# Performance work log

Hardware: AMD Instinct MI355X
Metric: run time of the kernel (lower is better)

Reference implementation:

```python
import jax, jax.numpy as jnp
import numpy as np

V, E, H, B, T = 50257, 300, 512, 4, 512  # vocab, embed(300 fixed), hid_size, batch, max_seq_len


def setup_inputs() -> dict:
    key = jax.random.key(0)
    ks = jax.random.split(key, 12)
    n = lambda k, shp, s: jax.random.normal(k, shp, dtype=jnp.float32) * s
    return {
        "tokens": jax.random.randint(ks[0], (B, T), 0, V),
        "emb_table": n(ks[1], (V, E), 0.02),      # frozen pretrained embedding
        # forward-direction LstmCellWithProjection params (cell_size == hidden_size == H)
        "W_ih_f": n(ks[2], (E, 4 * H), 0.05),     # input_linearity (no bias)
        "W_hh_f": n(ks[3], (H, 4 * H), 0.05),     # state_linearity weight
        "b_f": jnp.zeros((4 * H,), jnp.float32),  # state_linearity bias
        "W_proj_f": n(ks[4], (H, H), 0.05),       # state_projection (no bias)
        # backward direction
        "W_ih_b": n(ks[5], (E, 4 * H), 0.05),
        "W_hh_b": n(ks[6], (H, 4 * H), 0.05),
        "b_b": jnp.zeros((4 * H,), jnp.float32),
        "W_proj_b": n(ks[7], (H, H), 0.05),
        # final vocab projection nn.Linear(H, V)
        "W_lin": n(ks[8], (H, V), 0.02),
        "b_lin": jnp.zeros((V,), jnp.float32),
    }


def _lstm_proj_scan(x, W_ih, W_hh, b, W_proj):
    """ElmoLstm's LstmCellWithProjection over time. x: [B,T,E] -> [B,T,H]."""
    xp = jnp.einsum("bte,eg->btg", x, W_ih)  # precompute input projections [B,T,4H]

    def step(carry, xt):  # xt: [B,4H]
        h, c = carry
        p = xt + h @ W_hh + b
        i = jax.nn.sigmoid(p[:, :H])
        f = jax.nn.sigmoid(p[:, H:2 * H])
        g = jnp.tanh(p[:, 2 * H:3 * H])
        o = jax.nn.sigmoid(p[:, 3 * H:])
        c2 = i * g + f * c
        h2 = (o * jnp.tanh(c2)) @ W_proj  # projected hidden state
        return (h2, c2), h2

    init = (jnp.zeros((x.shape[0], H), x.dtype), jnp.zeros((x.shape[0], H), x.dtype))
    _, hs = jax.lax.scan(step, init, jnp.swapaxes(xp, 0, 1))  # [T,B,H]
    return jnp.swapaxes(hs, 0, 1)  # [B,T,H]


def reference(tokens, emb_table, W_ih_f, W_hh_f, b_f, W_proj_f,
              W_ih_b, W_hh_b, b_b, W_proj_b, W_lin, b_lin):
    x = emb_table[tokens]  # embedding gather [B,T,E]
    fwd = _lstm_proj_scan(x, W_ih_f, W_hh_f, b_f, W_proj_f)
    bwd = _lstm_proj_scan(x[:, ::-1], W_ih_b, W_hh_b, b_b, W_proj_b)[:, ::-1]
    # num_layers == 1 -> enc is (1,B,T,2H); fwd half / bwd half each through shared Linear
    logits_fwd = (fwd @ W_lin + b_lin).reshape(-1, V)  # [B*T, V]
    logits_bwd = (bwd @ W_lin + b_lin).reshape(-1, V)
    return jnp.concatenate([logits_fwd, logits_bwd], axis=0)  # [2*B*T, V]
```

## Files before the change

kernel.cpp:

```cpp
#include <hip/hip_runtime.h>
#include <hip/hip_bf16.h>

typedef unsigned short u16;
typedef unsigned int u32;
typedef unsigned long long u64;
typedef short bf16x8 __attribute__((ext_vector_type(8)));
typedef float f32x4 __attribute__((ext_vector_type(4)));

#define AS1C(p) ((const __attribute__((address_space(1))) void*)(p))
#define AS3(p)  ((__attribute__((address_space(3))) void*)(p))

__device__ __forceinline__ u16 f2bf(float f) {
    union { float f; unsigned u; } v; v.f = f;
    unsigned x = v.u;
    unsigned r = (x + 0x7FFFu + ((x >> 16) & 1u)) >> 16;
    return (u16)r;
}

__device__ __forceinline__ void tpose_dev(float (*tile)[33],
        const float* __restrict__ in, u16* __restrict__ out,
        int R, int C, int outR, int ldO, int bx, int by) {
    int c0 = bx * 32, r0 = by * 32;
    int tx = threadIdx.x & 31, ty = threadIdx.x >> 5;
#pragma unroll
    for (int yy = 0; yy < 4; ++yy) {
        int r = r0 + ty + yy * 8, cc = c0 + tx;
        tile[ty + yy * 8][tx] = (r < R && cc < C) ? in[(size_t)r * C + cc] : 0.f;
    }
    __syncthreads();
#pragma unroll
    for (int yy = 0; yy < 4; ++yy) {
        int c = c0 + ty + yy * 8, r = r0 + tx;
        if (c < outR && r < ldO) out[(size_t)c * ldO + r] = f2bf(tile[tx][ty + yy * 8]);
    }
}

__global__ __launch_bounds__(256) void prep(
    const int* __restrict__ tokens, const float* __restrict__ emb, u16* __restrict__ xemb,
    const float* __restrict__ W_ih_f, u16* __restrict__ WT_ihf,
    const float* __restrict__ W_ih_b, u16* __restrict__ WT_ihb,
    const float* __restrict__ W_hh_f, u16* __restrict__ WT_hhf,
    const float* __restrict__ W_hh_b, u16* __restrict__ WT_hhb,
    const float* __restrict__ W_proj_f, u16* __restrict__ WprojTf,
    const float* __restrict__ W_proj_b, u16* __restrict__ WprojTb,
    u16* __restrict__ WprojAf, u16* __restrict__ WprojAb,
    u64* __restrict__ htag)
{
    __shared__ float tile[32][33];
    int bid = blockIdx.x;
    int tid = threadIdx.x;
    if (bid < 2048) {
        int tok = tokens[bid];
        const float* src = emb + (size_t)tok * 300;
        u16* dst = xemb + (size_t)bid * 320;
        int c = tid;
        if (c < 320) dst[c] = (c < 300) ? f2bf(src[c]) : (u16)0;
        c += 256;
        if (c < 320) dst[c] = (c < 300) ? f2bf(src[c]) : (u16)0;
        return;
    }
    bid -= 2048;
    if (bid < 640)  { tpose_dev(tile, W_ih_f, WT_ihf, 300, 2048, 2048, 320, bid % 64, bid / 64); return; }
    bid -= 640;
    if (bid < 640)  { tpose_dev(tile, W_ih_b, WT_ihb, 300, 2048, 2048, 320, bid % 64, bid / 64); return; }
    bid -= 640;
    if (bid < 1024) { tpose_dev(tile, W_hh_f, WT_hhf, 512, 2048, 2048, 512, bid % 64, bid / 64); return; }
    bid -= 1024;
    if (bid < 1024) { tpose_dev(tile, W_hh_b, WT_hhb, 512, 2048, 2048, 512, bid % 64, bid / 64); return; }
    bid -= 1024;
    if (bid < 256)  { tpose_dev(tile, W_proj_f, WprojTf, 512, 512, 512, 512, bid % 16, bid / 16); return; }
    bid -= 256;
    if (bid < 256)  { tpose_dev(tile, W_proj_b, WprojTb, 512, 512, 512, 512, bid % 16, bid / 16); return; }
    bid -= 256;
    if (bid < 512)  { int i = bid * 512 + tid; WprojAf[i] = f2bf(W_proj_f[i]); WprojAf[i + 256] = f2bf(W_proj_f[i + 256]); return; }
    bid -= 512;
    if (bid < 512)  { int i = bid * 512 + tid; WprojAb[i] = f2bf(W_proj_b[i]); WprojAb[i + 256] = f2bf(W_proj_b[i + 256]); return; }
    bid -= 512;
    for (int i = tid; i < 2 * 2 * 4 * 256; i += 256) htag[i] = 0ull;
}

struct GemmJob {
    const u16* A; const u16* BT; float* Cf; u16* Cb; const float* bias;
    int M, Nreal, K, ldA, ldB, ldC, arev, orev, orow_base;
};

__device__ __forceinline__ void gemm_body(const GemmJob& j) {
    __shared__ char As[8192];
    __shared__ char Bs[8192];
    const int tid = threadIdx.x;
    const int lane = tid & 63;
    const int wid = tid >> 6;
    const int wr = wid >> 1, wc = wid & 1;
    const int m0 = blockIdx.y * 128;
    const int n0 = blockIdx.x * 128;

    f32x4 zero4 = {0.f, 0.f, 0.f, 0.f};
    f32x4 acc[4][4];
#pragma unroll
    for (int i = 0; i < 4; ++i)
#pragma unroll
        for (int jx = 0; jx < 4; ++jx) acc[i][jx] = zero4;

    const int kIters = j.K >> 5;
    const int l15 = lane & 15, kg = lane >> 4;

    const int srow0 = wid * 32 + (lane >> 2);
    const int srow1 = srow0 + 16;
    const int c0 = (lane & 3) ^ (srow0 & 3);
    const int c1 = (lane & 3) ^ (srow1 & 3);
    int ar0 = m0 + srow0, ar1 = m0 + srow1;
    if (j.arev) {
        ar0 = (ar0 & ~511) | (511 - (ar0 & 511));
        ar1 = (ar1 & ~511) | (511 - (ar1 & 511));
    }
    const u16* ga0 = j.A + (size_t)ar0 * j.ldA + c0 * 8;
    const u16* ga1 = j.A + (size_t)ar1 * j.ldA + c1 * 8;
    const u16* gb0 = j.BT + (size_t)(n0 + srow0) * j.ldB + c0 * 8;
    const u16* gb1 = j.BT + (size_t)(n0 + srow1) * j.ldB + c1 * 8;
    char* ldsA0 = As + wid * 2048;
    char* ldsA1 = As + wid * 2048 + 1024;
    char* ldsB0 = Bs + wid * 2048;
    char* ldsB1 = Bs + wid * 2048 + 1024;

    for (int kt = 0; kt < kIters; ++kt) {
        const int k0 = kt * 32;
        __builtin_amdgcn_global_load_lds(AS1C(ga0 + k0), AS3(ldsA0), 16, 0, 0);
        __builtin_amdgcn_global_load_lds(AS1C(ga1 + k0), AS3(ldsA1), 16, 0, 0);
        __builtin_amdgcn_global_load_lds(AS1C(gb0 + k0), AS3(ldsB0), 16, 0, 0);
        __builtin_amdgcn_global_load_lds(AS1C(gb1 + k0), AS3(ldsB1), 16, 0, 0);
        __syncthreads();

        bf16x8 af[4], bfr[4];
#pragma unroll
        for (int mt = 0; mt < 4; ++mt) {
            int r = wr * 64 + mt * 16 + l15;
            af[mt] = *(const bf16x8*)(As + r * 64 + ((kg ^ (r & 3)) * 16));
        }
#pragma unroll
        for (int nt = 0; nt < 4; ++nt) {
            int r = wc * 64 + nt * 16 + l15;
            bfr[nt] = *(const bf16x8*)(Bs + r * 64 + ((kg ^ (r & 3)) * 16));
        }
#pragma unroll
        for (int mt = 0; mt < 4; ++mt)
#pragma unroll
            for (int nt = 0; nt < 4; ++nt)
                acc[mt][nt] = __builtin_amdgcn_mfma_f32_16x16x32_bf16(af[mt], bfr[nt], acc[mt][nt], 0, 0, 0);
        __syncthreads();
    }

#pragma unroll
    for (int nt = 0; nt < 4; ++nt) {
        int col = n0 + wc * 64 + nt * 16 + l15;
        float bv = (j.bias != nullptr && col < j.Nreal) ? j.bias[col] : 0.f;
#pragma unroll
        for (int mt = 0; mt < 4; ++mt) {
#pragma unroll
            for (int jx = 0; jx < 4; ++jx) {
                int m = m0 + wr * 64 + mt * 16 + kg * 4 + jx;
                int om = j.orev ? ((m & ~511) | (511 - (m & 511))) : m;
                om += j.orow_base;
                if (col < j.Nreal) {
                    float v = acc[mt][nt][jx] + bv;
                    if (j.Cf) j.Cf[(size_t)om * j.ldC + col] = v;
                    else      j.Cb[(size_t)om * j.ldC + col] = f2bf(v);
                }
            }
        }
    }
}

__global__ __launch_bounds__(256) void gemm_multi4(GemmJob j0, GemmJob j1, GemmJob j2, GemmJob j3) {
    GemmJob j = (blockIdx.z == 0) ? j0 : (blockIdx.z == 1) ? j1 : (blockIdx.z == 2) ? j2 : j3;
    if ((int)blockIdx.y * 128 >= j.M) return;
    gemm_body(j);
}
__global__ __launch_bounds__(256) void gemm_multi2(GemmJob j0, GemmJob j1) {
    GemmJob j = blockIdx.z ? j1 : j0;
    gemm_body(j);
}
__global__ __launch_bounds__(256) void gemm_one(GemmJob j0) { gemm_body(j0); }

__global__ __launch_bounds__(256) void lstm_fused(
    const float* __restrict__ Wc_f, const float* __restrict__ Wc_b,
    const float* __restrict__ xp_f, const float* __restrict__ xp_b,
    u64* __restrict__ htag,
    u16* __restrict__ hpre_f, u16* __restrict__ hpre_b,
    const float* __restrict__ W_lin, u16* __restrict__ WT_lin)
{
    __shared__ float tile[32][33];
    __shared__ u16 hlds[4][520];
    __shared__ float gsum[4][4][16];
    __shared__ float cbuf[4][16];

    if (blockIdx.x >= 64) {
        int job = blockIdx.x - 64;
        tpose_dev(tile, W_lin, WT_lin, 512, 50257, 50304, 512, job % 1572, job / 1572);
        return;
    }
    __builtin_amdgcn_s_setprio(1);

    const int tid = threadIdx.x;
    const int dir = blockIdx.x >> 5;
    const int blk = blockIdx.x & 31;
    const int lane = tid & 63;
    const int wid = tid >> 6;
    const int l15 = lane & 15;
    const int kg = lane >> 4;

    const float* wcsrc = dir ? Wc_b : Wc_f;
    const float* xp    = dir ? xp_b : xp_f;
    u16* hpre          = dir ? hpre_b : hpre_f;
    u64* ht            = htag + (size_t)dir * 2 * 4 * 256;

    bf16x8 wcf[16];
#pragma unroll
    for (int ks = 0; ks < 16; ++ks) {
        bf16x8 w;
#pragma unroll
        for (int e = 0; e < 8; ++e) {
            int k = ks * 32 + kg * 8 + e;
            w[e] = (short)f2bf(wcsrc[(size_t)k * 2048 + wid * 512 + blk * 16 + l15]);
        }
        wcf[ks] = w;
    }
    if (tid < 64) cbuf[tid >> 4][tid & 15] = 0.f;
    __syncthreads();

    const bf16x8 zero8 = {0, 0, 0, 0, 0, 0, 0, 0};
    const int b = tid >> 4, hu = tid & 15;

    for (int t = 0; t < 512; ++t) {
        float xpv0 = 0.f, xpv1 = 0.f, xpv2 = 0.f, xpv3 = 0.f;
        if (tid < 64) {
            const float* xr = xp + ((size_t)(b * 512 + t)) * 2048 + blk * 16 + hu;
            xpv0 = xr[0]; xpv1 = xr[512]; xpv2 = xr[1024]; xpv3 = xr[1536];
        }
        {
            const u64* src = ht + (size_t)(t & 1) * 4 * 256;
            const u64* p0 = src + tid;
            const u64* p1 = src + 256 + tid;
            const u64* p2 = src + 512 + tid;
            const u64* p3 = src + 768 + tid;
            const u32 target = (u32)t;
            u64 w0, w1, w2, w3;
            for (;;) {
                asm volatile(
                    "global_load_dwordx2 %0, %4, off sc0 sc1\n\t"
                    "global_load_dwordx2 %1, %5, off sc0 sc1\n\t"
                    "global_load_dwordx2 %2, %6, off sc0 sc1\n\t"
                    "global_load_dwordx2 %3, %7, off sc0 sc1\n\t"
                    "s_waitcnt vmcnt(0)"
                    : "=&v"(w0), "=&v"(w1), "=&v"(w2), "=&v"(w3)
                    : "v"(p0), "v"(p1), "v"(p2), "v"(p3)
                    : "memory");
                if (((u32)(w0 >> 32) == target) & ((u32)(w1 >> 32) == target) &
                    ((u32)(w2 >> 32) == target) & ((u32)(w3 >> 32) == target)) break;
                __builtin_amdgcn_s_sleep(1);
            }
            asm volatile("" ::: "memory");
            *(u32*)&hlds[0][tid * 2] = (u32)w0;
            *(u32*)&hlds[1][tid * 2] = (u32)w1;
            *(u32*)&hlds[2][tid * 2] = (u32)w2;
            *(u32*)&hlds[3][tid * 2] = (u32)w3;
        }
        __syncthreads();

        f32x4 a0 = {0,0,0,0}, a1 = {0,0,0,0}, a2 = {0,0,0,0}, a3 = {0,0,0,0};
#pragma unroll
        for (int ks = 0; ks < 16; ++ks) {
            bf16x8 a = zero8;
            if (l15 < 4) a = *(const bf16x8*)&hlds[l15][ks * 32 + kg * 8];
            switch (ks & 3) {
                case 0: a0 = __builtin_amdgcn_mfma_f32_16x16x32_bf16(a, wcf[ks], a0, 0, 0, 0); break;
                case 1: a1 = __builtin_amdgcn_mfma_f32_16x16x32_bf16(a, wcf[ks], a1, 0, 0, 0); break;
                case 2: a2 = __builtin_amdgcn_mfma_f32_16x16x32_bf16(a, wcf[ks], a2, 0, 0, 0); break;
                default: a3 = __builtin_amdgcn_mfma_f32_16x16x32_bf16(a, wcf[ks], a3, 0, 0, 0); break;
            }
        }
        f32x4 accs = (a0 + a1) + (a2 + a3);
        if (lane < 16) {
#pragma unroll
            for (int jx = 0; jx < 4; ++jx) gsum[wid][jx][lane] = accs[jx];
        }
        __syncthreads();

        if (tid < 64) {
            float pi = xpv0 + gsum[0][b][hu];
            float pf = xpv1 + gsum[1][b][hu];
            float pg = xpv2 + gsum[2][b][hu];
            float po = xpv3 + gsum[3][b][hu];
            float iv = 1.f / (1.f + expf(-pi));
            float fv = 1.f / (1.f + expf(-pf));
            float gv = tanhf(pg);
            float ov = 1.f / (1.f + expf(-po));
            float c2 = iv * gv + fv * cbuf[b][hu];
            cbuf[b][hu] = c2;
            u16 hpb = f2bf(ov * tanhf(c2));
            unsigned v = hpb;
            unsigned nb = (unsigned)__shfl_down((int)v, 1);
            if ((tid & 1) == 0) {
                u32 packed = v | (nb << 16);
                u64 val = ((u64)(u32)(t + 1) << 32) | (u64)packed;
                size_t idx = (size_t)(((t + 1) & 1) * 4 + b) * 256 + blk * 8 + (hu >> 1);
                __hip_atomic_store(&ht[idx], val, __ATOMIC_RELAXED, __HIP_MEMORY_SCOPE_AGENT);
            }
            hpre[(size_t)(b * 512 + t) * 512 + blk * 16 + hu] = hpb;
        }
    }
}

extern "C" void kernel_launch(void* const* d_in, const int* in_sizes, int n_in,
                              void* d_out, int out_size, void* d_ws, size_t ws_size,
                              hipStream_t stream) {
    const int*   tokens   = (const int*)d_in[0];
    const float* emb      = (const float*)d_in[1];
    const float* W_ih_f   = (const float*)d_in[2];
    const float* W_hh_f   = (const float*)d_in[3];
    const float* b_f      = (const float*)d_in[4];
    const float* W_proj_f = (const float*)d_in[5];
    const float* W_ih_b   = (const float*)d_in[6];
    const float* W_hh_b   = (const float*)d_in[7];
    const float* b_b      = (const float*)d_in[8];
    const float* W_proj_b = (const float*)d_in[9];
    const float* W_lin    = (const float*)d_in[10];
    const float* b_lin    = (const float*)d_in[11];
    float* out = (float*)d_out;

    char* ws = (char*)d_ws;
    size_t off = 0;
    auto alloc = [&](size_t bytes) -> char* {
        char* p = ws + off;
        off = (off + bytes + 255) & ~(size_t)255;
        return p;
    };
    u16* xemb     = (u16*)alloc(2048 * 320 * 2);
    u16* WT_ihf   = (u16*)alloc(2048 * 320 * 2);
    u16* WT_ihb   = (u16*)alloc(2048 * 320 * 2);
    u16* WT_hhf   = (u16*)alloc(2048 * 512 * 2);
    u16* WT_hhb   = (u16*)alloc(2048 * 512 * 2);
    u16* WprojTf  = (u16*)alloc(512 * 512 * 2);
    u16* WprojTb  = (u16*)alloc(512 * 512 * 2);
    u16* WprojAf  = (u16*)alloc(512 * 512 * 2);
    u16* WprojAb  = (u16*)alloc(512 * 512 * 2);
    u16* WT_lin   = (u16*)alloc((size_t)50304 * 512 * 2);
    float* xpf    = (float*)alloc((size_t)2048 * 2048 * 4);
    float* xpb    = (float*)alloc((size_t)2048 * 2048 * 4);
    float* Wc32f  = (float*)alloc((size_t)512 * 2048 * 4);
    float* Wc32b  = (float*)alloc((size_t)512 * 2048 * 4);
    u16* hpref    = (u16*)alloc((size_t)2048 * 512 * 2);
    u16* hpreb    = (u16*)alloc((size_t)2048 * 512 * 2);
    u16* hall     = (u16*)alloc((size_t)4096 * 512 * 2);
    u64* htag     = (u64*)alloc((size_t)2 * 2 * 4 * 256 * 8);

    prep<<<6913, 256, 0, stream>>>(tokens, emb, xemb,
                                   W_ih_f, WT_ihf, W_ih_b, WT_ihb,
                                   W_hh_f, WT_hhf, W_hh_b, WT_hhb,
                                   W_proj_f, WprojTf, W_proj_b, WprojTb,
                                   WprojAf, WprojAb, htag);

    GemmJob jxf = {xemb, WT_ihf, xpf, nullptr, b_f, 2048, 2048, 320, 320, 320, 2048, 0, 0, 0};
    GemmJob jxb = {xemb, WT_ihb, xpb, nullptr, b_b, 2048, 2048, 320, 320, 320, 2048, 1, 0, 0};
    GemmJob jwf = {WprojAf, WT_hhf, Wc32f, nullptr, nullptr, 512, 2048, 512, 512, 512, 2048, 0, 0, 0};
    GemmJob jwb = {WprojAb, WT_hhb, Wc32b, nullptr, nullptr, 512, 2048, 512, 512, 512, 2048, 0, 0, 0};
    gemm_multi4<<<dim3(16, 16, 4), 256, 0, stream>>>(jxf, jxb, jwf, jwb);

    lstm_fused<<<64 + 1572 * 16, 256, 0, stream>>>(Wc32f, Wc32b, xpf, xpb, htag,
                                                   hpref, hpreb, W_lin, WT_lin);

    GemmJob jpf = {hpref, WprojTf, nullptr, hall, nullptr, 2048, 512, 512, 512, 512, 512, 0, 0, 0};
    GemmJob jpb = {hpreb, WprojTb, nullptr, hall, nullptr, 2048, 512, 512, 512, 512, 512, 0, 1, 2048};
    gemm_multi2<<<dim3(4, 16, 2), 256, 0, stream>>>(jpf, jpb);

    GemmJob jl = {hall, WT_lin, out, nullptr, b_lin, 4096, 50257, 512, 512, 512, 50257, 0, 0, 0};
    gemm_one<<<dim3(393, 32), 256, 0, stream>>>(jl);
}
```

Baseline: 1.793 ms.

## Fuse projection and vocab GEMMs into LSTM kernel with counter-based dataflow overlap

Merges the hidden-projection GEMM and the large vocab-projection GEMM into the persistent LSTM launch. Progress counters let projection tiles start as soon as 128-step chunks of the recurrence finish, and vocab tiles start as soon as their row bands are projected. The goal is to overlap the large output GEMM with the serial recurrence and remove two kernel launches. It also coarsens the W_lin transpose to one block per column strip, writing with packed atomic stores. This relies on spin-waiting blocks and on the LSTM blocks being resident first, so it risks deadlock or slowed recurrence if waiting blocks take compute-unit slots or memory bandwidth the recurrence needs.

```diff
diff --git a/kernel.cpp b/kernel.cpp
--- a/kernel.cpp
+++ b/kernel.cpp
@@ -16,10 +16,16 @@
     unsigned r = (x + 0x7FFFu + ((x >> 16) & 1u)) >> 16;
     return (u16)r;
 }
+__device__ __forceinline__ void st_atomic_u32(u32* p, u32 v) {
+    __hip_atomic_store(p, v, __ATOMIC_RELAXED, __HIP_MEMORY_SCOPE_AGENT);
+}
+__device__ __forceinline__ u32 ld_atomic_u32(const u32* p) {
+    return __hip_atomic_load(p, __ATOMIC_RELAXED, __HIP_MEMORY_SCOPE_AGENT);
+}
 
 __device__ __forceinline__ void tpose_dev(float (*tile)[33],
         const float* __restrict__ in, u16* __restrict__ out,
-        int R, int C, int outR, int ldO, int bx, int by) {
+        int R, int C, int outR, int ldO, int bx, int by, int atomicStore) {
     int c0 = bx * 32, r0 = by * 32;
     int tx = threadIdx.x & 31, ty = threadIdx.x >> 5;
 #pragma unroll
@@ -31,8 +37,16 @@
 #pragma unroll
     for (int yy = 0; yy < 4; ++yy) {
         int c = c0 + ty + yy * 8, r = r0 + tx;
-        if (c < outR && r < ldO) out[(size_t)c * ldO + r] = f2bf(tile[tx][ty + yy * 8]);
-    }
+        float v = tile[tx][ty + yy * 8];
+        if (atomicStore) {
+            float pv = __shfl_down(v, 1);
+            if ((tx & 1) == 0 && c < outR && r < ldO)
+                st_atomic_u32((u32*)&out[(size_t)c * ldO + r], (u32)f2bf(v) | ((u32)f2bf(pv) << 16));
+        } else {
+            if (c < outR && r < ldO) out[(size_t)c * ldO + r] = f2bf(v);
+        }
+    }
+    __syncthreads();
 }
 
 __global__ __launch_bounds__(256) void prep(
@@ -44,7 +58,7 @@
     const float* __restrict__ W_proj_f, u16* __restrict__ WprojTf,
     const float* __restrict__ W_proj_b, u16* __restrict__ WprojTb,
     u16* __restrict__ WprojAf, u16* __restrict__ WprojAb,
-    u64* __restrict__ htag)
+    u64* __restrict__ htag, u32* __restrict__ ctr)
 {
     __shared__ float tile[32][33];
     int bid = blockIdx.x;
@@ -60,23 +74,23 @@
         return;
     }
     bid -= 2048;
-    if (bid < 640)  { tpose_dev(tile, W_ih_f, WT_ihf, 300, 2048, 2048, 320, bid % 64, bid / 64); return; }
+    if (bid < 640)  { tpose_dev(tile, W_ih_f, WT_ihf, 300, 2048, 2048, 320, bid % 64, bid / 64, 0); return; }
     bid -= 640;
-    if (bid < 640)  { tpose_dev(tile, W_ih_b, WT_ihb, 300, 2048, 2048, 320, bid % 64, bid / 64); return; }
+    if (bid < 640)  { tpose_dev(tile, W_ih_b, WT_ihb, 300, 2048, 2048, 320, bid % 64, bid / 64, 0); return; }
     bid -= 640;
-    if (bid < 1024) { tpose_dev(tile, W_hh_f, WT_hhf, 512, 2048, 2048, 512, bid % 64, bid / 64); return; }
+    if (bid < 1024) { tpose_dev(tile, W_hh_f, WT_hhf, 512, 2048, 2048, 512, bid % 64, bid / 64, 0); return; }
     bid -= 1024;
-    if (bid < 1024) { tpose_dev(tile, W_hh_b, WT_hhb, 512, 2048, 2048, 512, bid % 64, bid / 64); return; }
+    if (bid < 1024) { tpose_dev(tile, W_hh_b, WT_hhb, 512, 2048, 2048, 512, bid % 64, bid / 64, 0); return; }
     bid -= 1024;
-    if (bid < 256)  { tpose_dev(tile, W_proj_f, WprojTf, 512, 512, 512, 512, bid % 16, bid / 16); return; }
+    if (bid < 256)  { tpose_dev(tile, W_proj_f, WprojTf, 512, 512, 512, 512, bid % 16, bid / 16, 0); return; }
     bid -= 256;
-    if (bid < 256)  { tpose_dev(tile, W_proj_b, WprojTb, 512, 512, 512, 512, bid % 16, bid / 16); return; }
+    if (bid < 256)  { tpose_dev(tile, W_proj_b, WprojTb, 512, 512, 512, 512, bid % 16, bid / 16, 0); return; }
     bid -= 256;
     if (bid < 512)  { int i = bid * 512 + tid; WprojAf[i] = f2bf(W_proj_f[i]); WprojAf[i + 256] = f2bf(W_proj_f[i + 256]); return; }
     bid -= 512;
     if (bid < 512)  { int i = bid * 512 + tid; WprojAb[i] = f2bf(W_proj_b[i]); WprojAb[i + 256] = f2bf(W_proj_b[i + 256]); return; }
-    bid -= 512;
     for (int i = tid; i < 2 * 2 * 4 * 256; i += 256) htag[i] = 0ull;
+    if (tid < 64) ctr[tid] = 0;
 }
 
 struct GemmJob {
@@ -84,15 +98,12 @@
     int M, Nreal, K, ldA, ldB, ldC, arev, orev, orow_base;
 };
 
-__device__ __forceinline__ void gemm_body(const GemmJob& j) {
-    __shared__ char As[8192];
-    __shared__ char Bs[8192];
+__device__ __forceinline__ void gemm_body(const GemmJob& j, int m0, int n0,
+                                          char* As, char* Bs, int atomicCb) {
     const int tid = threadIdx.x;
     const int lane = tid & 63;
     const int wid = tid >> 6;
     const int wr = wid >> 1, wc = wid & 1;
-    const int m0 = blockIdx.y * 128;
-    const int n0 = blockIdx.x * 128;
 
     f32x4 zero4 = {0.f, 0.f, 0.f, 0.f};
     f32x4 acc[4][4];
@@ -160,8 +171,13 @@
                 int m = m0 + wr * 64 + mt * 16 + kg * 4 + jx;
                 int om = j.orev ? ((m & ~511) | (511 - (m & 511))) : m;
                 om += j.orow_base;
-                if (col < j.Nreal) {
-                    float v = acc[mt][nt][jx] + bv;
+                float v = acc[mt][nt][jx] + bv;
+                if (atomicCb) {
+                    float pv = __shfl_down(v, 1);
+                    if ((l15 & 1) == 0 && col < j.Nreal)
+                        st_atomic_u32((u32*)(j.Cb + (size_t)om * j.ldC + col),
+                                      (u32)f2bf(v) | ((u32)f2bf(pv) << 16));
+                } else if (col < j.Nreal) {
                     if (j.Cf) j.Cf[(size_t)om * j.ldC + col] = v;
                     else      j.Cb[(size_t)om * j.ldC + col] = f2bf(v);
                 }
@@ -171,36 +187,77 @@
 }
 
 __global__ __launch_bounds__(256) void gemm_multi4(GemmJob j0, GemmJob j1, GemmJob j2, GemmJob j3) {
+    __shared__ char pool[16384];
     GemmJob j = (blockIdx.z == 0) ? j0 : (blockIdx.z == 1) ? j1 : (blockIdx.z == 2) ? j2 : j3;
     if ((int)blockIdx.y * 128 >= j.M) return;
-    gemm_body(j);
-}
-__global__ __launch_bounds__(256) void gemm_multi2(GemmJob j0, GemmJob j1) {
-    GemmJob j = blockIdx.z ? j1 : j0;
-    gemm_body(j);
-}
-__global__ __launch_bounds__(256) void gemm_one(GemmJob j0) { gemm_body(j0); }
+    gemm_body(j, blockIdx.y * 128, blockIdx.x * 128, pool, pool + 8192, 0);
+}
 
 __global__ __launch_bounds__(256) void lstm_fused(
     const float* __restrict__ Wc_f, const float* __restrict__ Wc_b,
     const float* __restrict__ xp_f, const float* __restrict__ xp_b,
     u64* __restrict__ htag,
     u16* __restrict__ hpre_f, u16* __restrict__ hpre_b,
-    const float* __restrict__ W_lin, u16* __restrict__ WT_lin)
+    const float* __restrict__ W_lin, u16* __restrict__ WT_lin,
+    const u16* __restrict__ WprojTf, const u16* __restrict__ WprojTb,
+    u16* __restrict__ hall, const float* __restrict__ b_lin,
+    float* __restrict__ out, u32* __restrict__ ctr)
 {
-    __shared__ float tile[32][33];
-    __shared__ u16 hlds[4][520];
-    __shared__ float gsum[4][4][16];
-    __shared__ float cbuf[4][16];
-
-    if (blockIdx.x >= 64) {
-        int job = blockIdx.x - 64;
-        tpose_dev(tile, W_lin, WT_lin, 512, 50257, 50304, 512, job % 1572, job / 1572);
-        return;
-    }
+    __shared__ char pool[16640];
+    const int tid = threadIdx.x;
+    int bid = blockIdx.x;
+
+    if (bid >= 64) {
+        bid -= 64;
+        if (bid < 1572) {
+            float (*tile)[33] = (float(*)[33])pool;
+            for (int by = 0; by < 16; ++by)
+                tpose_dev(tile, W_lin, WT_lin, 512, 50257, 50304, 512, bid, by, 1);
+            asm volatile("s_waitcnt vmcnt(0)" ::: "memory");
+            __syncthreads();
+            if (tid == 0) __hip_atomic_fetch_add(&ctr[0], 1u, __ATOMIC_RELAXED, __HIP_MEMORY_SCOPE_AGENT);
+            return;
+        }
+        bid -= 1572;
+        if (bid < 128) {
+            int dir = bid >> 6, r = bid & 63, y = r >> 2, x = r & 3;
+            int m0 = y * 128, n0 = x * 128;
+            if (tid == 0) {
+                while (ld_atomic_u32(&ctr[8 + dir * 4 + (y & 3)]) < 32u) __builtin_amdgcn_s_sleep(16);
+            }
+            __syncthreads();
+            GemmJob j = { dir ? hpre_b : hpre_f, dir ? WprojTb : WprojTf, nullptr, hall, nullptr,
+                          2048, 512, 512, 512, 512, 512, 0, dir ? 1 : 0, dir ? 2048 : 0 };
+            gemm_body(j, m0, n0, pool, pool + 8192, 1);
+            asm volatile("s_waitcnt vmcnt(0)" ::: "memory");
+            __syncthreads();
+            if (tid == 0) {
+                int obrow = j.orow_base + (j.orev ? ((m0 & ~511) | (511 - ((m0 + 127) & 511))) : m0);
+                __hip_atomic_fetch_add(&ctr[16 + (obrow >> 7)], 1u, __ATOMIC_RELAXED, __HIP_MEMORY_SCOPE_AGENT);
+            }
+            return;
+        }
+        bid -= 128;
+        {
+            int cid = bid / (393 * 8), rr = bid % (393 * 8), bi = rr / 393, x = rr % 393;
+            int band = (bi < 4) ? (bi * 4 + cid) : (16 + (bi - 4) * 4 + (3 - cid));
+            if (tid == 0) {
+                while (ld_atomic_u32(&ctr[0]) < 1572u) __builtin_amdgcn_s_sleep(32);
+                while (ld_atomic_u32(&ctr[16 + band]) < 4u) __builtin_amdgcn_s_sleep(32);
+            }
+            __syncthreads();
+            GemmJob j = { hall, WT_lin, out, nullptr, b_lin,
+                          4096, 50257, 512, 512, 512, 50257, 0, 0, 0 };
+            gemm_body(j, band * 128, x * 128, pool, pool + 8192, 0);
+            return;
+        }
+    }
+
     __builtin_amdgcn_s_setprio(1);
-
-    const int tid = threadIdx.x;
+    u16 (*hlds)[520] = (u16(*)[520])pool;
+    float (*gsum)[4][16] = (float(*)[4][16])(pool + 4160);
+    float (*cbuf)[16] = (float(*)[16])(pool + 5184);
+
     const int dir = blockIdx.x >> 5;
     const int blk = blockIdx.x & 31;
     const int lane = tid & 63;
@@ -304,8 +361,14 @@
                 u64 val = ((u64)(u32)(t + 1) << 32) | (u64)packed;
                 size_t idx = (size_t)(((t + 1) & 1) * 4 + b) * 256 + blk * 8 + (hu >> 1);
                 __hip_atomic_store(&ht[idx], val, __ATOMIC_RELAXED, __HIP_MEMORY_SCOPE_AGENT);
-            }
-            hpre[(size_t)(b * 512 + t) * 512 + blk * 16 + hu] = hpb;
+                st_atomic_u32((u32*)&hpre[(size_t)(b * 512 + t) * 512 + blk * 16 + hu], packed);
+            }
+        }
+        if ((t & 127) == 127) {
+            if (tid < 64) { asm volatile("s_waitcnt vmcnt(0)" ::: "memory"); }
+            if (tid == 0)
+                __hip_atomic_fetch_add(&ctr[8 + dir * 4 + (t >> 7)], 1u,
+                                       __ATOMIC_RELAXED, __HIP_MEMORY_SCOPE_AGENT);
         }
     }
 }
@@ -352,12 +415,13 @@
     u16* hpreb    = (u16*)alloc((size_t)2048 * 512 * 2);
     u16* hall     = (u16*)alloc((size_t)4096 * 512 * 2);
     u64* htag     = (u64*)alloc((size_t)2 * 2 * 4 * 256 * 8);
+    u32* ctr      = (u32*)alloc(64 * 4);
 
     prep<<<6913, 256, 0, stream>>>(tokens, emb, xemb,
                                    W_ih_f, WT_ihf, W_ih_b, WT_ihb,
                                    W_hh_f, WT_hhf, W_hh_b, WT_hhb,
                                    W_proj_f, WprojTf, W_proj_b, WprojTb,
-                                   WprojAf, WprojAb, htag);
+                                   WprojAf, WprojAb, htag, ctr);
 
     GemmJob jxf = {xemb, WT_ihf, xpf, nullptr, b_f, 2048, 2048, 320, 320, 320, 2048, 0, 0, 0};
     GemmJob jxb = {xemb, WT_ihb, xpb, nullptr, b_b, 2048, 2048, 320, 320, 320, 2048, 1, 0, 0};
@@ -365,13 +429,7 @@
     GemmJob jwb = {WprojAb, WT_hhb, Wc32b, nullptr, nullptr, 512, 2048, 512, 512, 512, 2048, 0, 0, 0};
     gemm_multi4<<<dim3(16, 16, 4), 256, 0, stream>>>(jxf, jxb, jwf, jwb);
 
-    lstm_fused<<<64 + 1572 * 16, 256, 0, stream>>>(Wc32f, Wc32b, xpf, xpb, htag,
-                                                   hpref, hpreb, W_lin, WT_lin);
-
-    GemmJob jpf = {hpref, WprojTf, nullptr, hall, nullptr, 2048, 512, 512, 512, 512, 512, 0, 0, 0};
-    GemmJob jpb = {hpreb, WprojTb, nullptr, hall, nullptr, 2048, 512, 512, 512, 512, 512, 0, 1, 2048};
-    gemm_multi2<<<dim3(4, 16, 2), 256, 0, stream>>>(jpf, jpb);
-
-    GemmJob jl = {hall, WT_lin, out, nullptr, b_lin, 4096, 50257, 512, 512, 512, 50257, 0, 0, 0};
-    gemm_one<<<dim3(393, 32), 256, 0, stream>>>(jl);
-}
+    lstm_fused<<<64 + 1572 + 128 + 12576, 256, 0, stream>>>(
+        Wc32f, Wc32b, xpf, xpb, htag, hpref, hpreb,
+        W_lin, WT_lin, WprojTf, WprojTb, hall, b_lin, out, ctr);
+}
```

Measured after the change: 1.672 ms. 1.07x faster.
